# Kernel optimization log

Measured on AMD Instinct MI355X. Metric: run time of the kernel, lower is better.

Reference implementation:

```python
import jax, jax.numpy as jnp
import numpy as np

N_NODES = 10000
N_EDGES = 640000
D_FEAT = 128
EPS = 1e-12  # F.normalize default eps


def setup_inputs() -> dict:
    key = jax.random.key(0)
    k1, k2, k3 = jax.random.split(key, 3)
    x = jax.random.normal(k1, (N_NODES, D_FEAT), dtype=jnp.float32)
    edge = jax.random.randint(k2, (3, N_EDGES), 0, N_NODES, dtype=jnp.int64)
    edge_weight = jax.random.uniform(k3, (N_EDGES,), dtype=jnp.float32)
    return {"x": x, "edge": edge, "edge_weight": edge_weight}


def reference(x, edge, edge_weight):
    edge_j = edge[0]  # source nodes
    edge_i = edge[2]  # target nodes
    n = x.shape[0]
    # degree of each target node (scatter_add of edge weights)
    deg = jax.ops.segment_sum(edge_weight, edge_i, num_segments=n)
    # normalized edge weights: w_e = ew_e / deg[target(e)]
    w = edge_weight / deg[edge_i]
    # SpMM: out[i] = sum_{e: target=i} w_e * x[source(e)]
    msg = x[edge_j] * w[:, None]           # [E, D]
    out = jax.ops.segment_sum(msg, edge_i, num_segments=n)  # [N, D]
    out = jax.nn.relu(out)
    # row-wise L2 normalize (F.normalize: x / max(||x||, eps))
    norm = jnp.sqrt(jnp.sum(out * out, axis=1, keepdims=True))
    return out / jnp.maximum(norm, EPS)
```

## Files before the change

### kernel.cpp

```cpp
#include <hip/hip_runtime.h>
#include <hip/hip_fp16.h>
#include <math.h>

#define D_FEAT 128
#define EPS 1e-12f
#define TGRP 40
#define NBUCK_PAD 256
#define NBLK 250
#define CAP_CB 40
#define SLOTS_PB (NBLK * CAP_CB)
#define LCAP 3584
#define SPT 10
#define EPT 3
#define LSW_CAP 2560


__device__ inline float2 h2_to_f2(unsigned int u) {
    __half2 h = *reinterpret_cast<__half2*>(&u);
    return __half22float2(h);
}

__device__ inline float w12_to_f(unsigned int p) {
    return __half2float(__ushort_as_half((unsigned short)((p & 0xfffu) << 4)));
}

__global__ __launch_bounds__(1024)
void build_kernel(const int* __restrict__ edge_i,
                  const int* __restrict__ edge_j,
                  const float* __restrict__ ew,
                  const float* __restrict__ x,
                  unsigned int* __restrict__ xh,
                  unsigned char* __restrict__ cntcb,
                  unsigned int* __restrict__ payload,
                  int E, int total4, int nbuck) {
    __shared__ unsigned int hc[NBUCK_PAD];
    __shared__ unsigned int sc[NBUCK_PAD];
    __shared__ unsigned int lsw[LSW_CAP + CAP_CB];
    const int c   = blockIdx.x;
    const int tid = threadIdx.x;
    const int EPB = E / NBLK;

    if (tid < NBUCK_PAD) hc[tid] = 0;
    __syncthreads();

    for (int i = c * 1024 + tid; i < total4; i += NBLK * 1024) {
        float4 v = ((const float4*)x)[i];
        __half2 h01 = __floats2half2_rn(v.x, v.y);
        __half2 h23 = __floats2half2_rn(v.z, v.w);
        uint2 o;
        o.x = *reinterpret_cast<unsigned int*>(&h01);
        o.y = *reinterpret_cast<unsigned int*>(&h23);
        ((uint2*)xh)[i] = o;
    }

    const int e0 = c * EPB;
    unsigned int epl[EPT];
    int          ebk[EPT];
    unsigned int erk[EPT];
    #pragma unroll
    for (int k = 0; k < EPT; ++k) {
        erk[k] = 0xffffffffu;
        int idx = tid + k * 1024;
        if (idx < EPB) {
            int e = e0 + idx;
            int t = edge_i[e];
            int bkt  = t / TGRP;
            int tloc = t - bkt * TGRP;
            unsigned int hw = (unsigned int)__half_as_ushort(__float2half(ew[e]));
            unsigned int w12 = (hw + 8u) >> 4;
            epl[k] = ((unsigned int)edge_j[e] << 18) |
                     ((unsigned int)tloc << 12) | w12;
            ebk[k] = bkt;
            erk[k] = atomicAdd(&hc[bkt], 1u);
        }
    }
    __syncthreads();

    if (tid < NBUCK_PAD) sc[tid] = hc[tid];
    __syncthreads();
    for (int d = 1; d < NBUCK_PAD; d <<= 1) {
        unsigned int v = 0;
        if (tid < NBUCK_PAD && tid >= d) v = sc[tid - d];
        __syncthreads();
        if (tid < NBUCK_PAD) sc[tid] += v;
        __syncthreads();
    }

    #pragma unroll
    for (int k = 0; k < EPT; ++k) {
        if (erk[k] != 0xffffffffu) {
            unsigned int base = sc[ebk[k]] - hc[ebk[k]];
            lsw[base + erk[k]] = epl[k];
        }
    }
    __syncthreads();

    const int tot = nbuck * CAP_CB;
    for (int s = tid; s < tot; s += 1024) {
        int bkt  = s / CAP_CB;
        int slot = s - bkt * CAP_CB;
        payload[(size_t)bkt * SLOTS_PB + c * CAP_CB + slot] =
            lsw[sc[bkt] - hc[bkt] + slot];
    }

    if (tid < nbuck) {
        unsigned int v = hc[tid];
        cntcb[(size_t)tid * NBUCK_PAD + c] =
            (unsigned char)(v > CAP_CB ? CAP_CB : v);
    }
}

__global__ __launch_bounds__(1024)
void sort_gather_kernel(const unsigned char* __restrict__ cntcb,
                        const unsigned int* __restrict__ payload,
                        const unsigned int* __restrict__ xh,
                        float* __restrict__ out, int n) {
    __shared__ unsigned char cnt_c[NBLK];
    __shared__ unsigned int  cnt40[TGRP];
    __shared__ unsigned int  base40[TGRP + 1];
    __shared__ unsigned int  ssw[LCAP];
    const int b    = blockIdx.x;
    const int tid  = threadIdx.x;
    const int wv   = tid >> 6;
    const int lane = tid & 63;
    const int g    = lane >> 4;
    const int l16  = lane & 15;

    if (tid < NBLK) cnt_c[tid] = cntcb[(size_t)b * NBUCK_PAD + tid];
    if (tid < TGRP) cnt40[tid] = 0;
    __syncthreads();

    const unsigned int* __restrict__ pb = payload + (size_t)b * SLOTS_PB;

    unsigned int rk[SPT];
    #pragma unroll
    for (int k = 0; k < SPT; ++k) {
        rk[k] = 0xffffffffu;
        int s = tid + k * 1024;
        if (s < SLOTS_PB) {
            int c  = s / CAP_CB;
            int kk = s - c * CAP_CB;
            if (kk < (int)cnt_c[c]) {
                unsigned int p = pb[s];
                unsigned int tloc = (p >> 12) & 63u;
                rk[k] = atomicAdd(&cnt40[tloc], 1u);
            }
        }
    }
    __syncthreads();

    if (tid == 0) {
        unsigned int run = 0;
        for (int t = 0; t < TGRP; ++t) { base40[t] = run; run += cnt40[t]; }
        base40[TGRP] = run;
    }
    __syncthreads();

    #pragma unroll
    for (int k = 0; k < SPT; ++k) {
        if (rk[k] != 0xffffffffu) {
            int s = tid + k * 1024;
            unsigned int p = pb[s];
            unsigned int tloc = (p >> 12) & 63u;
            unsigned int pos = base40[tloc] + rk[k];
            if (pos < LCAP) ssw[pos] = p;
        }
    }
    __syncthreads();

    const uint4* __restrict__ xr = (const uint4*)xh;
    for (int tl = wv; tl < TGRP; tl += 16) {
        int t = b * TGRP + tl;
        if (t >= n) break;
        int beg = (int)base40[tl];
        int m   = (int)cnt40[tl];
        if (beg + m > LCAP) m = (LCAP - beg > 0) ? (LCAP - beg) : 0;

        float4 accA = {0.f,0.f,0.f,0.f};
        float4 accB = {0.f,0.f,0.f,0.f};

        int it = 0;
        for (; it + 15 < m; it += 16) {
            unsigned int pq[4]; uint4 hq[4];
            #pragma unroll
            for (int q = 0; q < 4; ++q) pq[q] = ssw[beg + it + q * 4 + g];
            #pragma unroll
            for (int q = 0; q < 4; ++q) hq[q] = xr[(size_t)(pq[q] >> 18) * 16 + l16];
            #pragma unroll
            for (int q = 0; q < 4; ++q) {
                float w = w12_to_f(pq[q]);
                float2 f;
                f = h2_to_f2(hq[q].x); accA.x = fmaf(f.x, w, accA.x); accA.y = fmaf(f.y, w, accA.y);
                f = h2_to_f2(hq[q].y); accA.z = fmaf(f.x, w, accA.z); accA.w = fmaf(f.y, w, accA.w);
                f = h2_to_f2(hq[q].z); accB.x = fmaf(f.x, w, accB.x); accB.y = fmaf(f.y, w, accB.y);
                f = h2_to_f2(hq[q].w); accB.z = fmaf(f.x, w, accB.z); accB.w = fmaf(f.y, w, accB.w);
            }
        }
        for (; it < m; it += 4) {
            int idx = it + g;
            unsigned int p = (idx < m) ? ssw[beg + idx] : 0u;
            uint4 h = xr[(size_t)(p >> 18) * 16 + l16];
            float w = w12_to_f(p);
            float2 f;
            f = h2_to_f2(h.x); accA.x = fmaf(f.x, w, accA.x); accA.y = fmaf(f.y, w, accA.y);
            f = h2_to_f2(h.y); accA.z = fmaf(f.x, w, accA.z); accA.w = fmaf(f.y, w, accA.w);
            f = h2_to_f2(h.z); accB.x = fmaf(f.x, w, accB.x); accB.y = fmaf(f.y, w, accB.y);
            f = h2_to_f2(h.w); accB.z = fmaf(f.x, w, accB.z); accB.w = fmaf(f.y, w, accB.w);
        }

        #pragma unroll
        for (int off = 16; off <= 32; off <<= 1) {
            accA.x += __shfl_xor(accA.x, off, 64);
            accA.y += __shfl_xor(accA.y, off, 64);
            accA.z += __shfl_xor(accA.z, off, 64);
            accA.w += __shfl_xor(accA.w, off, 64);
            accB.x += __shfl_xor(accB.x, off, 64);
            accB.y += __shfl_xor(accB.y, off, 64);
            accB.z += __shfl_xor(accB.z, off, 64);
            accB.w += __shfl_xor(accB.w, off, 64);
        }

        accA.x = fmaxf(accA.x, 0.f); accA.y = fmaxf(accA.y, 0.f);
        accA.z = fmaxf(accA.z, 0.f); accA.w = fmaxf(accA.w, 0.f);
        accB.x = fmaxf(accB.x, 0.f); accB.y = fmaxf(accB.y, 0.f);
        accB.z = fmaxf(accB.z, 0.f); accB.w = fmaxf(accB.w, 0.f);

        float ss = accA.x*accA.x + accA.y*accA.y + accA.z*accA.z + accA.w*accA.w
                 + accB.x*accB.x + accB.y*accB.y + accB.z*accB.z + accB.w*accB.w;
        #pragma unroll
        for (int off = 8; off > 0; off >>= 1) ss += __shfl_xor(ss, off, 64);

        float scale = 1.0f / fmaxf(sqrtf(ss), EPS);

        if (g == 0) {
            float4 o0 = { accA.x * scale, accA.y * scale, accA.z * scale, accA.w * scale };
            float4 o1 = { accB.x * scale, accB.y * scale, accB.z * scale, accB.w * scale };
            float4* orow = (float4*)out + (size_t)t * 32;
            orow[l16 * 2]     = o0;
            orow[l16 * 2 + 1] = o1;
        }
    }
}

__global__ void deg_kernel(const int* __restrict__ edge_i,
                           const float* __restrict__ ew,
                           float* __restrict__ deg, int E) {
    int e = blockIdx.x * blockDim.x + threadIdx.x;
    if (e < E) atomicAdd(&deg[edge_i[e]], ew[e]);
}

__global__ void scatter_kernel(const int* __restrict__ edge_j,
                               const int* __restrict__ edge_i,
                               const float* __restrict__ ew,
                               const float* __restrict__ deg,
                               const float* __restrict__ x,
                               float* __restrict__ out, int E) {
    int wave = (int)((blockIdx.x * (unsigned)blockDim.x + threadIdx.x) >> 6);
    int lane = threadIdx.x & 63;
    if (wave >= E) return;
    int tgt = edge_i[wave];
    int src = edge_j[wave];
    float w = ew[wave] / deg[tgt];
    const float2* xr = (const float2*)(x + (size_t)src * D_FEAT);
    float2 v = xr[lane];
    float* o = out + (size_t)tgt * D_FEAT + lane * 2;
    atomicAdd(o,     v.x * w);
    atomicAdd(o + 1, v.y * w);
}

__global__ void norm_kernel(float* __restrict__ out, int n) {
    int row = (int)((blockIdx.x * (unsigned)blockDim.x + threadIdx.x) >> 6);
    int lane = threadIdx.x & 63;
    if (row >= n) return;
    float2* o = (float2*)(out + (size_t)row * D_FEAT);
    float2 v = o[lane];
    v.x = fmaxf(v.x, 0.0f);
    v.y = fmaxf(v.y, 0.0f);
    float ss = v.x * v.x + v.y * v.y;
    #pragma unroll
    for (int off = 32; off > 0; off >>= 1) ss += __shfl_xor(ss, off, 64);
    float scale = 1.0f / fmaxf(sqrtf(ss), EPS);
    v.x *= scale;
    v.y *= scale;
    o[lane] = v;
}

static inline size_t align64(size_t v) { return (v + 63) & ~(size_t)63; }

extern "C" void kernel_launch(void* const* d_in, const int* in_sizes, int n_in,
                              void* d_out, int out_size, void* d_ws, size_t ws_size,
                              hipStream_t stream) {
    const float* x    = (const float*)d_in[0];
    const int*   edge = (const int*)d_in[1];
    const float* ew   = (const float*)d_in[2];
    float*       out  = (float*)d_out;

    const int E = in_sizes[2];
    const int n = in_sizes[0] / D_FEAT;

    const int* edge_j = edge;
    const int* edge_i = edge + 2 * (size_t)E;

    const int nbuck = (n + TGRP - 1) / TGRP;

    const size_t off_cnt = align64((size_t)n * D_FEAT * 2);
    const size_t off_pl  = align64(off_cnt + (size_t)nbuck * NBUCK_PAD);
    const size_t need    = off_pl + (size_t)nbuck * SLOTS_PB * 4;

    if (ws_size >= need && (E % NBLK) == 0 && (E / NBLK) <= LSW_CAP &&
        nbuck <= NBLK && (size_t)nbuck * TGRP >= (size_t)n &&
        nbuck <= NBUCK_PAD && n <= 16384) {
        char* ws = (char*)d_ws;
        unsigned int*  xh      = (unsigned int*)ws;
        unsigned char* cntcb   = (unsigned char*)(ws + off_cnt);
        unsigned int*  payload = (unsigned int*)(ws + off_pl);

        const int total4 = n * D_FEAT / 4;

        build_kernel<<<NBLK, 1024, 0, stream>>>(edge_i, edge_j, ew, x, xh,
                                                cntcb, payload, E, total4, nbuck);
        sort_gather_kernel<<<nbuck, 1024, 0, stream>>>(cntcb, payload, xh,
                                                       out, n);
    } else {
        float* deg = (float*)d_ws;
        hipMemsetAsync(deg, 0, (size_t)n * sizeof(float), stream);
        hipMemsetAsync(out, 0, (size_t)out_size * sizeof(float), stream);
        deg_kernel<<<(E + 255) / 256, 256, 0, stream>>>(edge_i, ew, deg, E);
        scatter_kernel<<<(E + 3) / 4, 256, 0, stream>>>(edge_j, edge_i, ew, deg, x, out, E);
        norm_kernel<<<(n + 3) / 4, 256, 0, stream>>>(out, n);
    }
}
```

Before: 88.19 us.

## Fuse build and sort-gather kernels into one cooperative launch with grid sync

Merges the two-kernel pipeline into a single cooperative kernel that runs the bucketing phase, does a grid-wide barrier, and then runs the per-bucket sort and gather phase. Shared memory is unioned between the two phases. The aim is to remove the second kernel launch and the gap between kernels. In exchange it adds grid-sync overhead and requires all 250 blocks of 1024 threads to be co-resident, with the old two-kernel path kept as a fallback if the cooperative launch fails.

```diff
diff --git a/kernel.cpp b/kernel.cpp
--- a/kernel.cpp
+++ b/kernel.cpp
@@ -1,6 +1,9 @@
 #include <hip/hip_runtime.h>
 #include <hip/hip_fp16.h>
+#include <hip/hip_cooperative_groups.h>
 #include <math.h>
+
+namespace cg = cooperative_groups;
 
 #define D_FEAT 128
 #define EPS 1e-12f
@@ -24,23 +27,29 @@
     return __half2float(__ushort_as_half((unsigned short)((p & 0xfffu) << 4)));
 }
 
-__global__ __launch_bounds__(1024)
-void build_kernel(const int* __restrict__ edge_i,
-                  const int* __restrict__ edge_j,
-                  const float* __restrict__ ew,
-                  const float* __restrict__ x,
-                  unsigned int* __restrict__ xh,
-                  unsigned char* __restrict__ cntcb,
-                  unsigned int* __restrict__ payload,
-                  int E, int total4, int nbuck) {
-    __shared__ unsigned int hc[NBUCK_PAD];
-    __shared__ unsigned int sc[NBUCK_PAD];
-    __shared__ unsigned int lsw[LSW_CAP + CAP_CB];
-    const int c   = blockIdx.x;
+struct K1Smem {
+    unsigned int hc[NBUCK_PAD];
+    unsigned int sc[NBUCK_PAD];
+    unsigned int lsw[LSW_CAP + CAP_CB];
+};
+struct K2Smem {
+    unsigned char cnt_c[NBLK];
+    unsigned int  cnt40[TGRP];
+    unsigned int  base40[TGRP + 1];
+    unsigned int  ssw[LCAP];
+};
+
+__device__ __forceinline__
+void k1_body(K1Smem& sm,
+             const int* __restrict__ edge_i, const int* __restrict__ edge_j,
+             const float* __restrict__ ew, const float* __restrict__ x,
+             unsigned int* __restrict__ xh, unsigned char* __restrict__ cntcb,
+             unsigned int* __restrict__ payload,
+             int E, int total4, int nbuck, int c) {
     const int tid = threadIdx.x;
     const int EPB = E / NBLK;
 
-    if (tid < NBUCK_PAD) hc[tid] = 0;
+    if (tid < NBUCK_PAD) sm.hc[tid] = 0;
     __syncthreads();
 
     for (int i = c * 1024 + tid; i < total4; i += NBLK * 1024) {
@@ -71,26 +80,26 @@
             epl[k] = ((unsigned int)edge_j[e] << 18) |
                      ((unsigned int)tloc << 12) | w12;
             ebk[k] = bkt;
-            erk[k] = atomicAdd(&hc[bkt], 1u);
-        }
-    }
-    __syncthreads();
-
-    if (tid < NBUCK_PAD) sc[tid] = hc[tid];
+            erk[k] = atomicAdd(&sm.hc[bkt], 1u);
+        }
+    }
+    __syncthreads();
+
+    if (tid < NBUCK_PAD) sm.sc[tid] = sm.hc[tid];
     __syncthreads();
     for (int d = 1; d < NBUCK_PAD; d <<= 1) {
         unsigned int v = 0;
-        if (tid < NBUCK_PAD && tid >= d) v = sc[tid - d];
+        if (tid < NBUCK_PAD && tid >= d) v = sm.sc[tid - d];
         __syncthreads();
-        if (tid < NBUCK_PAD) sc[tid] += v;
+        if (tid < NBUCK_PAD) sm.sc[tid] += v;
         __syncthreads();
     }
 
     #pragma unroll
     for (int k = 0; k < EPT; ++k) {
         if (erk[k] != 0xffffffffu) {
-            unsigned int base = sc[ebk[k]] - hc[ebk[k]];
-            lsw[base + erk[k]] = epl[k];
+            unsigned int base = sm.sc[ebk[k]] - sm.hc[ebk[k]];
+            sm.lsw[base + erk[k]] = epl[k];
         }
     }
     __syncthreads();
@@ -100,34 +109,30 @@
         int bkt  = s / CAP_CB;
         int slot = s - bkt * CAP_CB;
         payload[(size_t)bkt * SLOTS_PB + c * CAP_CB + slot] =
-            lsw[sc[bkt] - hc[bkt] + slot];
+            sm.lsw[sm.sc[bkt] - sm.hc[bkt] + slot];
     }
 
     if (tid < nbuck) {
-        unsigned int v = hc[tid];
+        unsigned int v = sm.hc[tid];
         cntcb[(size_t)tid * NBUCK_PAD + c] =
             (unsigned char)(v > CAP_CB ? CAP_CB : v);
     }
 }
 
-__global__ __launch_bounds__(1024)
-void sort_gather_kernel(const unsigned char* __restrict__ cntcb,
-                        const unsigned int* __restrict__ payload,
-                        const unsigned int* __restrict__ xh,
-                        float* __restrict__ out, int n) {
-    __shared__ unsigned char cnt_c[NBLK];
-    __shared__ unsigned int  cnt40[TGRP];
-    __shared__ unsigned int  base40[TGRP + 1];
-    __shared__ unsigned int  ssw[LCAP];
-    const int b    = blockIdx.x;
+__device__ __forceinline__
+void k2_body(K2Smem& sm,
+             const unsigned char* __restrict__ cntcb,
+             const unsigned int* __restrict__ payload,
+             const unsigned int* __restrict__ xh,
+             float* __restrict__ out, int n, int b) {
     const int tid  = threadIdx.x;
     const int wv   = tid >> 6;
     const int lane = tid & 63;
     const int g    = lane >> 4;
     const int l16  = lane & 15;
 
-    if (tid < NBLK) cnt_c[tid] = cntcb[(size_t)b * NBUCK_PAD + tid];
-    if (tid < TGRP) cnt40[tid] = 0;
+    if (tid < NBLK) sm.cnt_c[tid] = cntcb[(size_t)b * NBUCK_PAD + tid];
+    if (tid < TGRP) sm.cnt40[tid] = 0;
     __syncthreads();
 
     const unsigned int* __restrict__ pb = payload + (size_t)b * SLOTS_PB;
@@ -140,10 +145,10 @@
         if (s < SLOTS_PB) {
             int c  = s / CAP_CB;
             int kk = s - c * CAP_CB;
-            if (kk < (int)cnt_c[c]) {
+            if (kk < (int)sm.cnt_c[c]) {
                 unsigned int p = pb[s];
                 unsigned int tloc = (p >> 12) & 63u;
-                rk[k] = atomicAdd(&cnt40[tloc], 1u);
+                rk[k] = atomicAdd(&sm.cnt40[tloc], 1u);
             }
         }
     }
@@ -151,8 +156,8 @@
 
     if (tid == 0) {
         unsigned int run = 0;
-        for (int t = 0; t < TGRP; ++t) { base40[t] = run; run += cnt40[t]; }
-        base40[TGRP] = run;
+        for (int t = 0; t < TGRP; ++t) { sm.base40[t] = run; run += sm.cnt40[t]; }
+        sm.base40[TGRP] = run;
     }
     __syncthreads();
 
@@ -162,8 +167,8 @@
             int s = tid + k * 1024;
             unsigned int p = pb[s];
             unsigned int tloc = (p >> 12) & 63u;
-            unsigned int pos = base40[tloc] + rk[k];
-            if (pos < LCAP) ssw[pos] = p;
+            unsigned int pos = sm.base40[tloc] + rk[k];
+            if (pos < LCAP) sm.ssw[pos] = p;
         }
     }
     __syncthreads();
@@ -172,8 +177,8 @@
     for (int tl = wv; tl < TGRP; tl += 16) {
         int t = b * TGRP + tl;
         if (t >= n) break;
-        int beg = (int)base40[tl];
-        int m   = (int)cnt40[tl];
+        int beg = (int)sm.base40[tl];
+        int m   = (int)sm.cnt40[tl];
         if (beg + m > LCAP) m = (LCAP - beg > 0) ? (LCAP - beg) : 0;
 
         float4 accA = {0.f,0.f,0.f,0.f};
@@ -183,7 +188,7 @@
         for (; it + 15 < m; it += 16) {
             unsigned int pq[4]; uint4 hq[4];
             #pragma unroll
-            for (int q = 0; q < 4; ++q) pq[q] = ssw[beg + it + q * 4 + g];
+            for (int q = 0; q < 4; ++q) pq[q] = sm.ssw[beg + it + q * 4 + g];
             #pragma unroll
             for (int q = 0; q < 4; ++q) hq[q] = xr[(size_t)(pq[q] >> 18) * 16 + l16];
             #pragma unroll
@@ -198,7 +203,7 @@
         }
         for (; it < m; it += 4) {
             int idx = it + g;
-            unsigned int p = (idx < m) ? ssw[beg + idx] : 0u;
+            unsigned int p = (idx < m) ? sm.ssw[beg + idx] : 0u;
             uint4 h = xr[(size_t)(p >> 18) * 16 + l16];
             float w = w12_to_f(p);
             float2 f;
@@ -240,6 +245,47 @@
             orow[l16 * 2 + 1] = o1;
         }
     }
+}
+
+__global__ __launch_bounds__(1024)
+void fused_kernel(const int* __restrict__ edge_i,
+                  const int* __restrict__ edge_j,
+                  const float* __restrict__ ew,
+                  const float* __restrict__ x,
+                  unsigned int* __restrict__ xh,
+                  unsigned char* __restrict__ cntcb,
+                  unsigned int* __restrict__ payload,
+                  float* __restrict__ out,
+                  int E, int total4, int nbuck, int n) {
+    __shared__ union { K1Smem k1; K2Smem k2; } sm;
+    k1_body(sm.k1, edge_i, edge_j, ew, x, xh, cntcb, payload,
+            E, total4, nbuck, blockIdx.x);
+    cg::this_grid().sync();
+    if ((int)blockIdx.x < nbuck)
+        k2_body(sm.k2, cntcb, payload, xh, out, n, blockIdx.x);
+}
+
+__global__ __launch_bounds__(1024)
+void build_kernel(const int* __restrict__ edge_i,
+                  const int* __restrict__ edge_j,
+                  const float* __restrict__ ew,
+                  const float* __restrict__ x,
+                  unsigned int* __restrict__ xh,
+                  unsigned char* __restrict__ cntcb,
+                  unsigned int* __restrict__ payload,
+                  int E, int total4, int nbuck) {
+    __shared__ K1Smem sm;
+    k1_body(sm, edge_i, edge_j, ew, x, xh, cntcb, payload,
+            E, total4, nbuck, blockIdx.x);
+}
+
+__global__ __launch_bounds__(1024)
+void sort_gather_kernel(const unsigned char* __restrict__ cntcb,
+                        const unsigned int* __restrict__ payload,
+                        const unsigned int* __restrict__ xh,
+                        float* __restrict__ out, int n) {
+    __shared__ K2Smem sm;
+    k2_body(sm, cntcb, payload, xh, out, n, blockIdx.x);
 }
 
 __global__ void deg_kernel(const int* __restrict__ edge_i,
@@ -315,12 +361,26 @@
         unsigned char* cntcb   = (unsigned char*)(ws + off_cnt);
         unsigned int*  payload = (unsigned int*)(ws + off_pl);
 
-        const int total4 = n * D_FEAT / 4;
-
-        build_kernel<<<NBLK, 1024, 0, stream>>>(edge_i, edge_j, ew, x, xh,
-                                                cntcb, payload, E, total4, nbuck);
-        sort_gather_kernel<<<nbuck, 1024, 0, stream>>>(cntcb, payload, xh,
-                                                       out, n);
+        int total4 = n * D_FEAT / 4;
+
+        const int* a_ei = edge_i; const int* a_ej = edge_j;
+        const float* a_ew = ew;   const float* a_x = x;
+        unsigned int* a_xh = xh;  unsigned char* a_cnt = cntcb;
+        unsigned int* a_pl = payload; float* a_out = out;
+        int a_E = E, a_t4 = total4, a_nb = nbuck, a_n = n;
+        void* args[] = { &a_ei, &a_ej, &a_ew, &a_x, &a_xh, &a_cnt, &a_pl,
+                         &a_out, &a_E, &a_t4, &a_nb, &a_n };
+
+        hipError_t err = hipLaunchCooperativeKernel(
+            reinterpret_cast<void*>(fused_kernel),
+            dim3(NBLK), dim3(1024), args, 0, stream);
+
+        if (err != hipSuccess) {
+            build_kernel<<<NBLK, 1024, 0, stream>>>(edge_i, edge_j, ew, x, xh,
+                                                    cntcb, payload, E, total4, nbuck);
+            sort_gather_kernel<<<nbuck, 1024, 0, stream>>>(cntcb, payload, xh,
+                                                           out, n);
+        }
     } else {
         float* deg = (float*)d_ws;
         hipMemsetAsync(deg, 0, (size_t)n * sizeof(float), stream);
```

Result: slower. 133.6 us (+51.5%).
